# Performance work log

Hardware: AMD Instinct MI355X
Metric: run time of the kernel (lower is better)

The kernel has to match this reference:

```python
import jax, jax.numpy as jnp
import numpy as np

B, S, E, H = 4, 2048, 256, 8
D = E // H
SCALE = D ** -0.5


def setup_inputs() -> dict:
    key = jax.random.key(0)
    k1, k2, k3, k4, k5, k6 = jax.random.split(key, 6)
    x = jax.random.normal(k1, (B, S, E), dtype=jnp.float32)
    lengths = jax.random.randint(k2, (B,), S // 4, S + 1)
    # binary prefix mask, as assumed by mask[i].sum() == valid length in the original
    mask = (jnp.arange(S)[None, :] < lengths[:, None]).astype(jnp.int32)
    w_std = 1.0 / np.sqrt(E)
    Wq = jax.random.normal(k3, (E, E), dtype=jnp.float32) * w_std
    Wk = jax.random.normal(k4, (E, E), dtype=jnp.float32) * w_std
    Wv = jax.random.normal(k5, (E, E), dtype=jnp.float32) * w_std
    Wo = jax.random.normal(k6, (E, E), dtype=jnp.float32) * w_std
    return {"x": x, "mask": mask, "Wq": Wq, "Wk": Wk, "Wv": Wv, "Wo": Wo}


def _scramble_pad(attn_i, L):
    # attn_i: [S, H, D] attention output for one sample; only query rows < L are used.
    # Faithful to torch: attn[:L] viewed as [H, L, D] (after transpose(1,2)) then
    # reshape(L, E), zero-padded to [S, E]. The reshape mixes heads in a
    # length-dependent way, reproduced here with integer index arithmetic.
    L_safe = jnp.maximum(L, 1)
    flat = jnp.arange(S * E)                     # flat index into [H, L, D] row-major
    h = jnp.minimum(flat // (L_safe * D), H - 1)
    rem = flat % (L_safe * D)
    s = rem // D
    d = rem % D
    valid = flat < L * E
    vals = attn_i[s, h, d]
    return jnp.where(valid, vals, 0.0).reshape(S, E)


def reference(x, mask, Wq, Wk, Wv, Wo):
    # projections (torch Linear, no bias: y = x @ W.T), split heads
    Q = (x @ Wq.T).reshape(B, S, H, D)
    K = (x @ Wk.T).reshape(B, S, H, D)
    V = (x @ Wv.T).reshape(B, S, H, D)
    scores = jnp.einsum("bqhd,bkhd->bhqk", Q, K) * SCALE
    key_valid = mask[:, None, None, :] > 0       # prefix key mask == per-sample varlen attn
    scores = jnp.where(key_valid, scores, -1e30)
    P = jax.nn.softmax(scores, axis=-1)
    attn = jnp.einsum("bhqk,bkhd->bqhd", P, V)   # [B, S, H, D]
    lengths = mask.sum(axis=1)
    padded = jax.vmap(_scramble_pad)(attn, lengths)  # [B, S, E]
    return padded @ Wo.T
```

## Files before the change

kernel.cpp:

```cpp
#include <hip/hip_runtime.h>
#include <cmath>

#define Bn 4
#define Sn 2048
#define En 256
#define Hn 8
#define Dn 32
#define KD 256
#define NS 4
#define CHUNK 512

static constexpr float SCALE_LOG2E = 0.25504210472155044f;

typedef _Float16 half4_t __attribute__((ext_vector_type(4)));
typedef _Float16 half8_t __attribute__((ext_vector_type(8)));
typedef float float4_t __attribute__((ext_vector_type(4)));

__global__ __launch_bounds__(256) void cvt_kernel(
    const float* __restrict__ Wq, const float* __restrict__ Wk,
    const float* __restrict__ Wv, const float* __restrict__ Wo,
    const int* __restrict__ mask, _Float16* __restrict__ Wh,
    int* __restrict__ len) {
  if (blockIdx.x == 128) {
    const int b = threadIdx.x >> 6, lane = threadIdx.x & 63;
    int s = 0;
    for (int i = lane; i < Sn; i += 64) s += mask[b * Sn + i];
#pragma unroll
    for (int off = 32; off > 0; off >>= 1) s += __shfl_down(s, off, 64);
    if (lane == 0) len[b] = s;
    return;
  }
  const size_t wi = ((size_t)blockIdx.x * 256 + threadIdx.x) * 8;
  const int w = (int)(wi >> 16);
  const size_t off = wi & 65535;
  const float* src = (w == 0) ? Wq : (w == 1) ? Wk : (w == 2) ? Wv : Wo;
  float4 a = *(const float4*)&src[off];
  float4 b2 = *(const float4*)&src[off + 4];
  half8_t h;
  h[0] = (_Float16)a.x;  h[1] = (_Float16)a.y;
  h[2] = (_Float16)a.z;  h[3] = (_Float16)a.w;
  h[4] = (_Float16)b2.x; h[5] = (_Float16)b2.y;
  h[6] = (_Float16)b2.z; h[7] = (_Float16)b2.w;
  *(half8_t*)&(Wh + (size_t)w * 65536)[off] = h;
}

__global__ __launch_bounds__(256) void qkv_gemm(
    const float* __restrict__ x, const _Float16* __restrict__ Wh,
    _Float16* __restrict__ Qh, _Float16* __restrict__ Kh,
    _Float16* __restrict__ Vt) {
  const int lane = threadIdx.x & 63;
  const int wv = threadIdx.x >> 6;
  const int quad = lane >> 4, l15 = lane & 15;
  const int fid = blockIdx.x + 12 * blockIdx.y;
  const int wl = (fid & 7) * 48 + (fid >> 3);
  const int nb = wl % 12, mb = wl / 12;
  const int n0 = nb * 64;
  const int mw = mb * 256 + wv * 64;

  float4_t C[4][4];
#pragma unroll
  for (int i = 0; i < 4; ++i)
#pragma unroll
    for (int j = 0; j < 4; ++j) C[i][j] = (float4_t){0.f, 0.f, 0.f, 0.f};

  for (int k0 = 0; k0 < KD; k0 += 32) {
    half8_t A[4], Bf[4];
#pragma unroll
    for (int i = 0; i < 4; ++i) {
      const float4* xp =
          (const float4*)&x[(size_t)(mw + 16 * i + l15) * KD + k0 + quad * 8];
      const float4 a0 = xp[0], a1 = xp[1];
      A[i][0] = (_Float16)a0.x; A[i][1] = (_Float16)a0.y;
      A[i][2] = (_Float16)a0.z; A[i][3] = (_Float16)a0.w;
      A[i][4] = (_Float16)a1.x; A[i][5] = (_Float16)a1.y;
      A[i][6] = (_Float16)a1.z; A[i][7] = (_Float16)a1.w;
    }
#pragma unroll
    for (int j = 0; j < 4; ++j)
      Bf[j] = *(const half8_t*)&Wh[(size_t)(n0 + 16 * j + l15) * KD + k0 + quad * 8];
#pragma unroll
    for (int i = 0; i < 4; ++i)
#pragma unroll
      for (int j = 0; j < 4; ++j)
        C[i][j] = __builtin_amdgcn_mfma_f32_16x16x32_f16(A[i], Bf[j], C[i][j], 0, 0, 0);
  }

  const int mat = n0 >> 8;
  if (mat < 2) {
    _Float16* dstH = mat ? Kh : Qh;
    const float scale = mat ? 1.0f : SCALE_LOG2E;
#pragma unroll
    for (int i = 0; i < 4; ++i)
#pragma unroll
      for (int j = 0; j < 4; ++j) {
        const int c = ((n0 + 16 * j) & 255) + l15;
        const int h = c >> 5, d = c & 31;
#pragma unroll
        for (int r = 0; r < 4; ++r) {
          const int m = mw + 16 * i + quad * 4 + r;
          const int b = m >> 11, s = m & (Sn - 1);
          dstH[((size_t)(b * Hn + h) * Sn + s) * Dn + d] =
              (_Float16)(C[i][j][r] * scale);
        }
      }
  } else {
#pragma unroll
    for (int i = 0; i < 4; ++i)
#pragma unroll
      for (int j = 0; j < 4; ++j) {
        const int c = ((n0 + 16 * j) & 255) + l15;
        const int h = c >> 5, d = c & 31;
        const int m = mw + 16 * i + quad * 4;
        const int b = m >> 11, s = m & (Sn - 1);
        half4_t hv;
#pragma unroll
        for (int r = 0; r < 4; ++r) hv[r] = (_Float16)C[i][j][r];
        *(half4_t*)&Vt[(size_t)(b * Hn + h) * (Sn * Dn) +
                       (size_t)(s >> 5) * 1024 + d * 32 + (s & 31)] = hv;
      }
  }
}

__global__ __launch_bounds__(256) void out_gemm(
    const _Float16* __restrict__ Ph, const _Float16* __restrict__ Woh,
    float* __restrict__ out) {
  const int lane = threadIdx.x & 63;
  const int wv = threadIdx.x >> 6;
  const int quad = lane >> 4, l15 = lane & 15;
  const int fid = blockIdx.x + 4 * blockIdx.y;
  const int wl = (fid & 7) * 16 + (fid >> 3);
  const int nb = wl % 4, mb = wl / 4;
  const int n0 = nb * 64;
  const int mw = mb * 256 + wv * 64;

  float4_t C[4][4];
#pragma unroll
  for (int i = 0; i < 4; ++i)
#pragma unroll
    for (int j = 0; j < 4; ++j) C[i][j] = (float4_t){0.f, 0.f, 0.f, 0.f};

  for (int k0 = 0; k0 < KD; k0 += 32) {
    half8_t A[4], Bf[4];
#pragma unroll
    for (int i = 0; i < 4; ++i)
      A[i] = *(const half8_t*)&Ph[(size_t)(mw + 16 * i + l15) * KD + k0 + quad * 8];
#pragma unroll
    for (int j = 0; j < 4; ++j)
      Bf[j] = *(const half8_t*)&Woh[(size_t)(n0 + 16 * j + l15) * KD + k0 + quad * 8];
#pragma unroll
    for (int i = 0; i < 4; ++i)
#pragma unroll
      for (int j = 0; j < 4; ++j)
        C[i][j] = __builtin_amdgcn_mfma_f32_16x16x32_f16(A[i], Bf[j], C[i][j], 0, 0, 0);
  }

#pragma unroll
  for (int i = 0; i < 4; ++i)
#pragma unroll
    for (int j = 0; j < 4; ++j)
#pragma unroll
      for (int r = 0; r < 4; ++r)
        out[(size_t)(mw + 16 * i + quad * 4 + r) * En + n0 + 16 * j + l15] =
            C[i][j][r];
}

__global__ __launch_bounds__(256) void attn_kernel(
    const _Float16* __restrict__ Qh, const _Float16* __restrict__ Kh,
    const _Float16* __restrict__ Vt, const int* __restrict__ len,
    _Float16* __restrict__ pacc, float* __restrict__ pl) {
  const int lid = blockIdx.x + 32 * (blockIdx.y + 8 * blockIdx.z);
  const int h = lid & 7;
  const int w = lid >> 3;
  const int b = w >> 5;
  const int inner = w & 31;
  const int split = inner & (NS - 1);
  const int qg = inner >> 2;

  const int L = len[b];
  const int lane = threadIdx.x & 63;
  const int wv = threadIdx.x >> 6;
  const int q0 = (qg * 4 + wv) * 64;
  if (q0 >= L) return;
  const int ks = split * CHUNK;
  if (ks >= L) return;
  const int ke = min(L, ks + CHUNK);

  const int quad = lane >> 4;
  const int l15 = lane & 15;
  const size_t bh = (size_t)(b * Hn + h) * Sn;
  const _Float16* Vt0 = &Vt[(size_t)(b * Hn + h) * (Sn * Dn)];

  half8_t qf[4];
#pragma unroll
  for (int t = 0; t < 4; ++t)
    qf[t] = *(const half8_t*)&Qh[(bh + q0 + 16 * t + l15) * Dn + quad * 8];

  float4_t o0[4], o1[4];
  float ll[4];
#pragma unroll
  for (int t = 0; t < 4; ++t) {
    o0[t] = (float4_t){0.f, 0.f, 0.f, 0.f};
    o1[t] = (float4_t){0.f, 0.f, 0.f, 0.f};
    ll[t] = 0.f;
  }

  const int vo0 = l15 * 32 + quad * 4;
  const int vo1 = (l15 + 16) * 32 + quad * 4;

  const _Float16* vt_c = &Vt0[(size_t)(ks >> 5) * 1024];
  half8_t kfc0 = *(const half8_t*)&Kh[(bh + ks + l15) * Dn + quad * 8];
  half8_t kfc1 = *(const half8_t*)&Kh[(bh + ks + 16 + l15) * Dn + quad * 8];
  half4_t v0c = *(const half4_t*)&vt_c[vo0];
  half4_t v1c = *(const half4_t*)&vt_c[vo1];
  half4_t v2c = *(const half4_t*)&vt_c[vo0 + 16];
  half4_t v3c = *(const half4_t*)&vt_c[vo1 + 16];

  const int r1 = (ks + 32 < ke) ? ks + 32 : ks;
  const _Float16* vt_1 = &Vt0[(size_t)(r1 >> 5) * 1024];
  half8_t kfn0 = *(const half8_t*)&Kh[(bh + r1 + l15) * Dn + quad * 8];
  half8_t kfn1 = *(const half8_t*)&Kh[(bh + r1 + 16 + l15) * Dn + quad * 8];
  half4_t v0n = *(const half4_t*)&vt_1[vo0];
  half4_t v1n = *(const half4_t*)&vt_1[vo1];
  half4_t v2n = *(const half4_t*)&vt_1[vo0 + 16];
  half4_t v3n = *(const half4_t*)&vt_1[vo1 + 16];

  for (int k0 = ks; k0 < ke; k0 += 32) {
    const int kp = k0 + 64;
    const int kn = (kp < ke) ? kp : ks;
    const _Float16* vt_t = &Vt0[(size_t)(kn >> 5) * 1024];
    const half8_t kft0 = *(const half8_t*)&Kh[(bh + kn + l15) * Dn + quad * 8];
    const half8_t kft1 = *(const half8_t*)&Kh[(bh + kn + 16 + l15) * Dn + quad * 8];
    const half4_t v0t = *(const half4_t*)&vt_t[vo0];
    const half4_t v1t = *(const half4_t*)&vt_t[vo1];
    const half4_t v2t = *(const half4_t*)&vt_t[vo0 + 16];
    const half4_t v3t = *(const half4_t*)&vt_t[vo1 + 16];

    __builtin_amdgcn_s_setprio(1);
    float4_t st0[4], st1[4];
#pragma unroll
    for (int t = 0; t < 4; ++t) {
      st0[t] = (float4_t){0.f, 0.f, 0.f, 0.f};
      st1[t] = (float4_t){0.f, 0.f, 0.f, 0.f};
      st0[t] = __builtin_amdgcn_mfma_f32_16x16x32_f16(kfc0, qf[t], st0[t], 0, 0, 0);
      st1[t] = __builtin_amdgcn_mfma_f32_16x16x32_f16(kfc1, qf[t], st1[t], 0, 0, 0);
    }

    if (k0 + 32 <= ke) {
#pragma unroll
      for (int t = 0; t < 4; ++t) {
        half4_t pf0, pf1;
#pragma unroll
        for (int r = 0; r < 4; ++r) {
          const float pa = __builtin_amdgcn_exp2f(st0[t][r]);
          const float pb = __builtin_amdgcn_exp2f(st1[t][r]);
          ll[t] += pa + pb;
          pf0[r] = (_Float16)pa;
          pf1[r] = (_Float16)pb;
        }
        o0[t] = __builtin_amdgcn_mfma_f32_16x16x16f16(pf0, v0c, o0[t], 0, 0, 0);
        o1[t] = __builtin_amdgcn_mfma_f32_16x16x16f16(pf0, v1c, o1[t], 0, 0, 0);
        o0[t] = __builtin_amdgcn_mfma_f32_16x16x16f16(pf1, v2c, o0[t], 0, 0, 0);
        o1[t] = __builtin_amdgcn_mfma_f32_16x16x16f16(pf1, v3c, o1[t], 0, 0, 0);
      }
    } else {
      const int ka = k0 + quad * 4, kb = k0 + 16 + quad * 4;
#pragma unroll
      for (int t = 0; t < 4; ++t) {
        half4_t pf0, pf1;
#pragma unroll
        for (int r = 0; r < 4; ++r) {
          const float pa = __builtin_amdgcn_exp2f((ka + r < ke) ? st0[t][r] : -3.0e38f);
          const float pb = __builtin_amdgcn_exp2f((kb + r < ke) ? st1[t][r] : -3.0e38f);
          ll[t] += pa + pb;
          pf0[r] = (_Float16)pa;
          pf1[r] = (_Float16)pb;
        }
        o0[t] = __builtin_amdgcn_mfma_f32_16x16x16f16(pf0, v0c, o0[t], 0, 0, 0);
        o1[t] = __builtin_amdgcn_mfma_f32_16x16x16f16(pf0, v1c, o1[t], 0, 0, 0);
        o0[t] = __builtin_amdgcn_mfma_f32_16x16x16f16(pf1, v2c, o0[t], 0, 0, 0);
        o1[t] = __builtin_amdgcn_mfma_f32_16x16x16f16(pf1, v3c, o1[t], 0, 0, 0);
      }
    }
    __builtin_amdgcn_s_setprio(0);
    kfc0 = kfn0; kfc1 = kfn1;
    v0c = v0n; v1c = v1n; v2c = v2n; v3c = v3n;
    kfn0 = kft0; kfn1 = kft1;
    v0n = v0t; v1n = v1t; v2n = v2t; v3n = v3t;
  }

#pragma unroll
  for (int t = 0; t < 4; ++t) {
    ll[t] += __shfl_xor(ll[t], 16);
    ll[t] += __shfl_xor(ll[t], 32);
  }

  const size_t idx0 = ((size_t)(b * Hn + h) * NS + split) * Sn + q0;
#pragma unroll
  for (int t = 0; t < 4; ++t) {
#pragma unroll
    for (int r = 0; r < 4; ++r) {
      _Float16* pp = &pacc[(idx0 + 16 * t + quad * 4 + r) * 32];
      pp[l15] = (_Float16)o0[t][r];
      pp[l15 + 16] = (_Float16)o1[t][r];
    }
  }
  if (quad == 0) {
#pragma unroll
    for (int t = 0; t < 4; ++t) pl[idx0 + 16 * t + l15] = ll[t];
  }
}

__global__ __launch_bounds__(256) void combine_kernel(const _Float16* __restrict__ pacc,
                                                      const float* __restrict__ pl,
                                                      const int* __restrict__ len,
                                                      _Float16* __restrict__ Ph) {
  const int b = blockIdx.z;
  const int L = len[b];
  if (blockIdx.y == Hn) {
    _Float16* base = Ph + (size_t)b * Sn * En;
    const size_t end = (size_t)Sn * En;
    const size_t stride = (size_t)gridDim.x * 256 * 8;
    half8_t z = {0, 0, 0, 0, 0, 0, 0, 0};
    for (size_t idx = (size_t)L * En + ((size_t)blockIdx.x * 256 + threadIdx.x) * 8;
         idx < end; idx += stride)
      *(half8_t*)&base[idx] = z;
    return;
  }
  const int h = blockIdx.y;
  const int q = blockIdx.x * 256 + threadIdx.x;
  if (q >= L) return;
  const size_t base = (size_t)(b * Hn + h) * NS * Sn;

  float T = 0.f;
  float o[32];
#pragma unroll
  for (int d = 0; d < 32; ++d) o[d] = 0.f;
#pragma unroll
  for (int sp = 0; sp < NS; ++sp) {
    if (sp * CHUNK < L) {
      T += pl[base + (size_t)sp * Sn + q];
      const half8_t* pp = (const half8_t*)&pacc[(base + (size_t)sp * Sn + q) * 32];
#pragma unroll
      for (int i = 0; i < 4; ++i) {
        half8_t v = pp[i];
#pragma unroll
        for (int t2 = 0; t2 < 8; ++t2) o[i * 8 + t2] += (float)v[t2];
      }
    }
  }
  const float inv = 1.0f / T;
  _Float16* dst = &Ph[(size_t)b * Sn * En + (size_t)h * L * Dn + (size_t)q * Dn];
#pragma unroll
  for (int i = 0; i < 4; ++i) {
    half8_t hv;
#pragma unroll
    for (int t2 = 0; t2 < 8; ++t2) hv[t2] = (_Float16)(o[i * 8 + t2] * inv);
    *(half8_t*)&dst[i * 8] = hv;
  }
}

extern "C" void kernel_launch(void* const* d_in, const int* in_sizes, int n_in,
                              void* d_out, int out_size, void* d_ws, size_t ws_size,
                              hipStream_t stream) {
  (void)in_sizes; (void)n_in; (void)out_size; (void)ws_size;
  const float* x  = (const float*)d_in[0];
  const int* mask = (const int*)d_in[1];
  const float* Wq = (const float*)d_in[2];
  const float* Wk = (const float*)d_in[3];
  const float* Wv = (const float*)d_in[4];
  const float* Wo = (const float*)d_in[5];
  float* out = (float*)d_out;

  float* wsf = (float*)d_ws;
  int* lengths = (int*)d_ws;
  const size_t BHSD = (size_t)Bn * Hn * Sn * Dn;
  _Float16* Wh = (_Float16*)(wsf + 64);
  _Float16* Qh = Wh + 4 * 65536;
  _Float16* Kh = Qh + BHSD;
  _Float16* Vt = Kh + BHSD;
  _Float16* Ph = Vt + BHSD;
  _Float16* pacc = Ph + BHSD;
  float* pl = (float*)(pacc + (size_t)Bn * Hn * NS * Sn * 32);

  cvt_kernel<<<dim3(129), 256, 0, stream>>>(Wq, Wk, Wv, Wo, mask, Wh, lengths);
  qkv_gemm<<<dim3(12, 32), 256, 0, stream>>>(x, Wh, Qh, Kh, Vt);
  attn_kernel<<<dim3((Sn / 256) * NS, Hn, Bn), 256, 0, stream>>>(
      Qh, Kh, Vt, lengths, pacc, pl);
  combine_kernel<<<dim3(Sn / 256, Hn + 1, Bn), 256, 0, stream>>>(
      pacc, pl, lengths, Ph);
  out_gemm<<<dim3(4, 32), 256, 0, stream>>>(Ph, Wh + 3 * 65536, out);
}
```

Baseline: 143.4 us.

## Stage K/V tiles through swizzled LDS shared by all waves via direct loads

The attention kernel now double-buffers each 32-key K and V tile in shared memory using global_load_lds. Each of the four waves loads one quarter of the tile, and all waves in the block then read the whole tile from LDS instead of each fetching it from global memory separately. The projection kernel writes K and Vt with an XOR swizzle so the LDS fragment reads avoid bank conflicts. Waves whose query rows lie past the valid length still take part in staging and barriers, which adds two block barriers per tile and some idle wave work.

Measured after the change: 143.0 us. About the same (-0.3%).

```diff
diff --git a/kernel.cpp b/kernel.cpp
--- a/kernel.cpp
+++ b/kernel.cpp
@@ -86,9 +86,7 @@
   }
 
   const int mat = n0 >> 8;
-  if (mat < 2) {
-    _Float16* dstH = mat ? Kh : Qh;
-    const float scale = mat ? 1.0f : SCALE_LOG2E;
+  if (mat == 0) {
 #pragma unroll
     for (int i = 0; i < 4; ++i)
 #pragma unroll
@@ -99,8 +97,24 @@
         for (int r = 0; r < 4; ++r) {
           const int m = mw + 16 * i + quad * 4 + r;
           const int b = m >> 11, s = m & (Sn - 1);
-          dstH[((size_t)(b * Hn + h) * Sn + s) * Dn + d] =
-              (_Float16)(C[i][j][r] * scale);
+          Qh[((size_t)(b * Hn + h) * Sn + s) * Dn + d] =
+              (_Float16)(C[i][j][r] * SCALE_LOG2E);
+        }
+      }
+  } else if (mat == 1) {
+#pragma unroll
+    for (int i = 0; i < 4; ++i)
+#pragma unroll
+      for (int j = 0; j < 4; ++j) {
+        const int c = ((n0 + 16 * j) & 255) + l15;
+        const int h = c >> 5, d = c & 31;
+        const int g = d >> 3, dl = d & 7;
+#pragma unroll
+        for (int r = 0; r < 4; ++r) {
+          const int m = mw + 16 * i + quad * 4 + r;
+          const int b = m >> 11, s = m & (Sn - 1);
+          Kh[((size_t)(b * Hn + h) * Sn + s) * Dn + ((g ^ (s & 3)) << 3) + dl] =
+              (_Float16)C[i][j][r];
         }
       }
   } else {
@@ -112,11 +126,12 @@
         const int h = c >> 5, d = c & 31;
         const int m = mw + 16 * i + quad * 4;
         const int b = m >> 11, s = m & (Sn - 1);
+        const int g = (((s & 31) >> 3) ^ (d & 3)) << 3;
         half4_t hv;
 #pragma unroll
         for (int r = 0; r < 4; ++r) hv[r] = (_Float16)C[i][j][r];
         *(half4_t*)&Vt[(size_t)(b * Hn + h) * (Sn * Dn) +
-                       (size_t)(s >> 5) * 1024 + d * 32 + (s & 31)] = hv;
+                       (size_t)(s >> 5) * 1024 + d * 32 + g + (s & 7)] = hv;
       }
   }
 }
@@ -177,23 +192,29 @@
   const int qg = inner >> 2;
 
   const int L = len[b];
+  const int ks = split * CHUNK;
+  if (ks >= L) return;
+  const int ke = min(L, ks + CHUNK);
+  const int nr = (ke - ks + 31) >> 5;
+
   const int lane = threadIdx.x & 63;
   const int wv = threadIdx.x >> 6;
   const int q0 = (qg * 4 + wv) * 64;
-  if (q0 >= L) return;
-  const int ks = split * CHUNK;
-  if (ks >= L) return;
-  const int ke = min(L, ks + CHUNK);
+  const bool act = (q0 < L);
 
   const int quad = lane >> 4;
   const int l15 = lane & 15;
   const size_t bh = (size_t)(b * Hn + h) * Sn;
   const _Float16* Vt0 = &Vt[(size_t)(b * Hn + h) * (Sn * Dn)];
 
+  __shared__ char smem[8192] __attribute__((aligned(128)));
+
   half8_t qf[4];
-#pragma unroll
-  for (int t = 0; t < 4; ++t)
-    qf[t] = *(const half8_t*)&Qh[(bh + q0 + 16 * t + l15) * Dn + quad * 8];
+  if (act) {
+#pragma unroll
+    for (int t = 0; t < 4; ++t)
+      qf[t] = *(const half8_t*)&Qh[(bh + q0 + 16 * t + l15) * Dn + quad * 8];
+  }
 
   float4_t o0[4], o1[4];
   float ll[4];
@@ -204,89 +225,94 @@
     ll[t] = 0.f;
   }
 
-  const int vo0 = l15 * 32 + quad * 4;
-  const int vo1 = (l15 + 16) * 32 + quad * 4;
-
-  const _Float16* vt_c = &Vt0[(size_t)(ks >> 5) * 1024];
-  half8_t kfc0 = *(const half8_t*)&Kh[(bh + ks + l15) * Dn + quad * 8];
-  half8_t kfc1 = *(const half8_t*)&Kh[(bh + ks + 16 + l15) * Dn + quad * 8];
-  half4_t v0c = *(const half4_t*)&vt_c[vo0];
-  half4_t v1c = *(const half4_t*)&vt_c[vo1];
-  half4_t v2c = *(const half4_t*)&vt_c[vo0 + 16];
-  half4_t v3c = *(const half4_t*)&vt_c[vo1 + 16];
-
-  const int r1 = (ks + 32 < ke) ? ks + 32 : ks;
-  const _Float16* vt_1 = &Vt0[(size_t)(r1 >> 5) * 1024];
-  half8_t kfn0 = *(const half8_t*)&Kh[(bh + r1 + l15) * Dn + quad * 8];
-  half8_t kfn1 = *(const half8_t*)&Kh[(bh + r1 + 16 + l15) * Dn + quad * 8];
-  half4_t v0n = *(const half4_t*)&vt_1[vo0];
-  half4_t v1n = *(const half4_t*)&vt_1[vo1];
-  half4_t v2n = *(const half4_t*)&vt_1[vo0 + 16];
-  half4_t v3n = *(const half4_t*)&vt_1[vo1 + 16];
-
-  for (int k0 = ks; k0 < ke; k0 += 32) {
-    const int kp = k0 + 64;
-    const int kn = (kp < ke) ? kp : ks;
-    const _Float16* vt_t = &Vt0[(size_t)(kn >> 5) * 1024];
-    const half8_t kft0 = *(const half8_t*)&Kh[(bh + kn + l15) * Dn + quad * 8];
-    const half8_t kft1 = *(const half8_t*)&Kh[(bh + kn + 16 + l15) * Dn + quad * 8];
-    const half4_t v0t = *(const half4_t*)&vt_t[vo0];
-    const half4_t v1t = *(const half4_t*)&vt_t[vo1];
-    const half4_t v2t = *(const half4_t*)&vt_t[vo0 + 16];
-    const half4_t v3t = *(const half4_t*)&vt_t[vo1 + 16];
-
-    __builtin_amdgcn_s_setprio(1);
-    float4_t st0[4], st1[4];
-#pragma unroll
-    for (int t = 0; t < 4; ++t) {
-      st0[t] = (float4_t){0.f, 0.f, 0.f, 0.f};
-      st1[t] = (float4_t){0.f, 0.f, 0.f, 0.f};
-      st0[t] = __builtin_amdgcn_mfma_f32_16x16x32_f16(kfc0, qf[t], st0[t], 0, 0, 0);
-      st1[t] = __builtin_amdgcn_mfma_f32_16x16x32_f16(kfc1, qf[t], st1[t], 0, 0, 0);
+  const int swK = (quad ^ (l15 & 3)) << 4;
+  const int gV0 = (((quad >> 1) ^ (l15 & 3)) << 4) + ((quad & 1) << 3);
+  const int gV2 = ((((quad >> 1) + 2) ^ (l15 & 3)) << 4) + ((quad & 1) << 3);
+
+#define STAGE(bufsel, kk)                                                      \
+  do {                                                                         \
+    const char* gK_ = (const char*)(Kh + (bh + (kk)) * Dn);                    \
+    const char* gV_ = (const char*)(Vt0 + (size_t)((kk) >> 5) * 1024);         \
+    const char* src_ = (wv < 2) ? (gK_ + wv * 1024) : (gV_ + (wv - 2) * 1024); \
+    __builtin_amdgcn_global_load_lds(                                          \
+        (const __attribute__((address_space(1))) void*)(src_ + lane * 16),     \
+        (__attribute__((address_space(3))) void*)&smem[(bufsel) * 4096 +       \
+                                                       wv * 1024],             \
+        16, 0, 0);                                                             \
+  } while (0)
+
+  STAGE(0, ks);
+  int cur = 0;
+
+  for (int r = 0; r < nr; ++r) {
+    const int k0 = ks + (r << 5);
+    const int kn = (k0 + 32 < ke) ? (k0 + 32) : ks;
+    STAGE(cur ^ 1, kn);
+    asm volatile("s_waitcnt vmcnt(1)" ::: "memory");
+    __builtin_amdgcn_s_barrier();
+
+    if (act) {
+      const char* sK = &smem[cur * 4096];
+      const char* sV = &smem[cur * 4096 + 2048];
+      const half8_t kfc0 = *(const half8_t*)&sK[l15 * 64 + swK];
+      const half8_t kfc1 = *(const half8_t*)&sK[(l15 + 16) * 64 + swK];
+      const half4_t v0c = *(const half4_t*)&sV[l15 * 64 + gV0];
+      const half4_t v1c = *(const half4_t*)&sV[(l15 + 16) * 64 + gV0];
+      const half4_t v2c = *(const half4_t*)&sV[l15 * 64 + gV2];
+      const half4_t v3c = *(const half4_t*)&sV[(l15 + 16) * 64 + gV2];
+
+      float4_t st0[4], st1[4];
+#pragma unroll
+      for (int t = 0; t < 4; ++t) {
+        st0[t] = (float4_t){0.f, 0.f, 0.f, 0.f};
+        st1[t] = (float4_t){0.f, 0.f, 0.f, 0.f};
+        st0[t] = __builtin_amdgcn_mfma_f32_16x16x32_f16(kfc0, qf[t], st0[t], 0, 0, 0);
+        st1[t] = __builtin_amdgcn_mfma_f32_16x16x32_f16(kfc1, qf[t], st1[t], 0, 0, 0);
+      }
+
+      if (k0 + 32 <= ke) {
+#pragma unroll
+        for (int t = 0; t < 4; ++t) {
+          half4_t pf0, pf1;
+#pragma unroll
+          for (int r2 = 0; r2 < 4; ++r2) {
+            const float pa = __builtin_amdgcn_exp2f(st0[t][r2]);
+            const float pb = __builtin_amdgcn_exp2f(st1[t][r2]);
+            ll[t] += pa + pb;
+            pf0[r2] = (_Float16)pa;
+            pf1[r2] = (_Float16)pb;
+          }
+          o0[t] = __builtin_amdgcn_mfma_f32_16x16x16f16(pf0, v0c, o0[t], 0, 0, 0);
+          o1[t] = __builtin_amdgcn_mfma_f32_16x16x16f16(pf0, v1c, o1[t], 0, 0, 0);
+          o0[t] = __builtin_amdgcn_mfma_f32_16x16x16f16(pf1, v2c, o0[t], 0, 0, 0);
+          o1[t] = __builtin_amdgcn_mfma_f32_16x16x16f16(pf1, v3c, o1[t], 0, 0, 0);
+        }
+      } else {
+        const int ka = k0 + quad * 4, kb = k0 + 16 + quad * 4;
+#pragma unroll
+        for (int t = 0; t < 4; ++t) {
+          half4_t pf0, pf1;
+#pragma unroll
+          for (int r2 = 0; r2 < 4; ++r2) {
+            const float pa = __builtin_amdgcn_exp2f((ka + r2 < ke) ? st0[t][r2] : -3.0e38f);
+            const float pb = __builtin_amdgcn_exp2f((kb + r2 < ke) ? st1[t][r2] : -3.0e38f);
+            ll[t] += pa + pb;
+            pf0[r2] = (_Float16)pa;
+            pf1[r2] = (_Float16)pb;
+          }
+          o0[t] = __builtin_amdgcn_mfma_f32_16x16x16f16(pf0, v0c, o0[t], 0, 0, 0);
+          o1[t] = __builtin_amdgcn_mfma_f32_16x16x16f16(pf0, v1c, o1[t], 0, 0, 0);
+          o0[t] = __builtin_amdgcn_mfma_f32_16x16x16f16(pf1, v2c, o0[t], 0, 0, 0);
+          o1[t] = __builtin_amdgcn_mfma_f32_16x16x16f16(pf1, v3c, o1[t], 0, 0, 0);
+        }
+      }
     }
-
-    if (k0 + 32 <= ke) {
-#pragma unroll
-      for (int t = 0; t < 4; ++t) {
-        half4_t pf0, pf1;
-#pragma unroll
-        for (int r = 0; r < 4; ++r) {
-          const float pa = __builtin_amdgcn_exp2f(st0[t][r]);
-          const float pb = __builtin_amdgcn_exp2f(st1[t][r]);
-          ll[t] += pa + pb;
-          pf0[r] = (_Float16)pa;
-          pf1[r] = (_Float16)pb;
-        }
-        o0[t] = __builtin_amdgcn_mfma_f32_16x16x16f16(pf0, v0c, o0[t], 0, 0, 0);
-        o1[t] = __builtin_amdgcn_mfma_f32_16x16x16f16(pf0, v1c, o1[t], 0, 0, 0);
-        o0[t] = __builtin_amdgcn_mfma_f32_16x16x16f16(pf1, v2c, o0[t], 0, 0, 0);
-        o1[t] = __builtin_amdgcn_mfma_f32_16x16x16f16(pf1, v3c, o1[t], 0, 0, 0);
-      }
-    } else {
-      const int ka = k0 + quad * 4, kb = k0 + 16 + quad * 4;
-#pragma unroll
-      for (int t = 0; t < 4; ++t) {
-        half4_t pf0, pf1;
-#pragma unroll
-        for (int r = 0; r < 4; ++r) {
-          const float pa = __builtin_amdgcn_exp2f((ka + r < ke) ? st0[t][r] : -3.0e38f);
-          const float pb = __builtin_amdgcn_exp2f((kb + r < ke) ? st1[t][r] : -3.0e38f);
-          ll[t] += pa + pb;
-          pf0[r] = (_Float16)pa;
-          pf1[r] = (_Float16)pb;
-        }
-        o0[t] = __builtin_amdgcn_mfma_f32_16x16x16f16(pf0, v0c, o0[t], 0, 0, 0);
-        o1[t] = __builtin_amdgcn_mfma_f32_16x16x16f16(pf0, v1c, o1[t], 0, 0, 0);
-        o0[t] = __builtin_amdgcn_mfma_f32_16x16x16f16(pf1, v2c, o0[t], 0, 0, 0);
-        o1[t] = __builtin_amdgcn_mfma_f32_16x16x16f16(pf1, v3c, o1[t], 0, 0, 0);
-      }
-    }
-    __builtin_amdgcn_s_setprio(0);
-    kfc0 = kfn0; kfc1 = kfn1;
-    v0c = v0n; v1c = v1n; v2c = v2n; v3c = v3n;
-    kfn0 = kft0; kfn1 = kft1;
-    v0n = v0t; v1n = v1t; v2n = v2t; v3n = v3t;
-  }
+    __builtin_amdgcn_s_barrier();
+    cur ^= 1;
+  }
+#undef STAGE
+
+  if (!act) return;
 
 #pragma unroll
   for (int t = 0; t < 4; ++t) {
```

## Process 64 keys per attention loop iteration with single-stage register prefetch

Applied to the files above, without the earlier changes.

The attention inner loop now handles two 32-key sub-blocks per iteration. It prefetches the next 64 keys' K and V fragments one iteration ahead, replacing the two-deep rotating prefetch of 32-key tiles. The s_setprio priority hints are removed. This halves loop overhead and register rotation per key but shortens the prefetch distance and may raise register pressure. The tail handling also now assumes the 64-key tile's second half is readable even when only partly valid.

New measurement: 138.0 us. 3.7% less time.

```diff
diff --git a/kernel.cpp b/kernel.cpp
--- a/kernel.cpp
+++ b/kernel.cpp
@@ -207,45 +207,45 @@
   const int vo0 = l15 * 32 + quad * 4;
   const int vo1 = (l15 + 16) * 32 + quad * 4;
 
-  const _Float16* vt_c = &Vt0[(size_t)(ks >> 5) * 1024];
+  const _Float16* vtA = &Vt0[(size_t)(ks >> 5) * 1024];
   half8_t kfc0 = *(const half8_t*)&Kh[(bh + ks + l15) * Dn + quad * 8];
   half8_t kfc1 = *(const half8_t*)&Kh[(bh + ks + 16 + l15) * Dn + quad * 8];
-  half4_t v0c = *(const half4_t*)&vt_c[vo0];
-  half4_t v1c = *(const half4_t*)&vt_c[vo1];
-  half4_t v2c = *(const half4_t*)&vt_c[vo0 + 16];
-  half4_t v3c = *(const half4_t*)&vt_c[vo1 + 16];
-
-  const int r1 = (ks + 32 < ke) ? ks + 32 : ks;
-  const _Float16* vt_1 = &Vt0[(size_t)(r1 >> 5) * 1024];
-  half8_t kfn0 = *(const half8_t*)&Kh[(bh + r1 + l15) * Dn + quad * 8];
-  half8_t kfn1 = *(const half8_t*)&Kh[(bh + r1 + 16 + l15) * Dn + quad * 8];
-  half4_t v0n = *(const half4_t*)&vt_1[vo0];
-  half4_t v1n = *(const half4_t*)&vt_1[vo1];
-  half4_t v2n = *(const half4_t*)&vt_1[vo0 + 16];
-  half4_t v3n = *(const half4_t*)&vt_1[vo1 + 16];
-
-  for (int k0 = ks; k0 < ke; k0 += 32) {
-    const int kp = k0 + 64;
-    const int kn = (kp < ke) ? kp : ks;
-    const _Float16* vt_t = &Vt0[(size_t)(kn >> 5) * 1024];
-    const half8_t kft0 = *(const half8_t*)&Kh[(bh + kn + l15) * Dn + quad * 8];
-    const half8_t kft1 = *(const half8_t*)&Kh[(bh + kn + 16 + l15) * Dn + quad * 8];
-    const half4_t v0t = *(const half4_t*)&vt_t[vo0];
-    const half4_t v1t = *(const half4_t*)&vt_t[vo1];
-    const half4_t v2t = *(const half4_t*)&vt_t[vo0 + 16];
-    const half4_t v3t = *(const half4_t*)&vt_t[vo1 + 16];
-
-    __builtin_amdgcn_s_setprio(1);
+  half8_t kfc2 = *(const half8_t*)&Kh[(bh + ks + 32 + l15) * Dn + quad * 8];
+  half8_t kfc3 = *(const half8_t*)&Kh[(bh + ks + 48 + l15) * Dn + quad * 8];
+  half4_t v0c = *(const half4_t*)&vtA[vo0];
+  half4_t v1c = *(const half4_t*)&vtA[vo1];
+  half4_t v2c = *(const half4_t*)&vtA[vo0 + 16];
+  half4_t v3c = *(const half4_t*)&vtA[vo1 + 16];
+  half4_t v4c = *(const half4_t*)&vtA[1024 + vo0];
+  half4_t v5c = *(const half4_t*)&vtA[1024 + vo1];
+  half4_t v6c = *(const half4_t*)&vtA[1024 + vo0 + 16];
+  half4_t v7c = *(const half4_t*)&vtA[1024 + vo1 + 16];
+
+  for (int k0 = ks; k0 < ke; k0 += 64) {
+    const int kn = (k0 + 64 < ke) ? k0 + 64 : ks;
+    const _Float16* vtN = &Vt0[(size_t)(kn >> 5) * 1024];
+    const half8_t kfn0 = *(const half8_t*)&Kh[(bh + kn + l15) * Dn + quad * 8];
+    const half8_t kfn1 = *(const half8_t*)&Kh[(bh + kn + 16 + l15) * Dn + quad * 8];
+    const half8_t kfn2 = *(const half8_t*)&Kh[(bh + kn + 32 + l15) * Dn + quad * 8];
+    const half8_t kfn3 = *(const half8_t*)&Kh[(bh + kn + 48 + l15) * Dn + quad * 8];
+    const half4_t v0n = *(const half4_t*)&vtN[vo0];
+    const half4_t v1n = *(const half4_t*)&vtN[vo1];
+    const half4_t v2n = *(const half4_t*)&vtN[vo0 + 16];
+    const half4_t v3n = *(const half4_t*)&vtN[vo1 + 16];
+    const half4_t v4n = *(const half4_t*)&vtN[1024 + vo0];
+    const half4_t v5n = *(const half4_t*)&vtN[1024 + vo1];
+    const half4_t v6n = *(const half4_t*)&vtN[1024 + vo0 + 16];
+    const half4_t v7n = *(const half4_t*)&vtN[1024 + vo1 + 16];
+
     float4_t st0[4], st1[4];
-#pragma unroll
-    for (int t = 0; t < 4; ++t) {
-      st0[t] = (float4_t){0.f, 0.f, 0.f, 0.f};
-      st1[t] = (float4_t){0.f, 0.f, 0.f, 0.f};
-      st0[t] = __builtin_amdgcn_mfma_f32_16x16x32_f16(kfc0, qf[t], st0[t], 0, 0, 0);
-      st1[t] = __builtin_amdgcn_mfma_f32_16x16x32_f16(kfc1, qf[t], st1[t], 0, 0, 0);
-    }
-
-    if (k0 + 32 <= ke) {
+    if (k0 + 64 <= ke) {
+#pragma unroll
+      for (int t = 0; t < 4; ++t) {
+        st0[t] = (float4_t){0.f, 0.f, 0.f, 0.f};
+        st1[t] = (float4_t){0.f, 0.f, 0.f, 0.f};
+        st0[t] = __builtin_amdgcn_mfma_f32_16x16x32_f16(kfc0, qf[t], st0[t], 0, 0, 0);
+        st1[t] = __builtin_amdgcn_mfma_f32_16x16x32_f16(kfc1, qf[t], st1[t], 0, 0, 0);
+      }
 #pragma unroll
       for (int t = 0; t < 4; ++t) {
         half4_t pf0, pf1;
@@ -262,8 +262,38 @@
         o0[t] = __builtin_amdgcn_mfma_f32_16x16x16f16(pf1, v2c, o0[t], 0, 0, 0);
         o1[t] = __builtin_amdgcn_mfma_f32_16x16x16f16(pf1, v3c, o1[t], 0, 0, 0);
       }
+#pragma unroll
+      for (int t = 0; t < 4; ++t) {
+        st0[t] = (float4_t){0.f, 0.f, 0.f, 0.f};
+        st1[t] = (float4_t){0.f, 0.f, 0.f, 0.f};
+        st0[t] = __builtin_amdgcn_mfma_f32_16x16x32_f16(kfc2, qf[t], st0[t], 0, 0, 0);
+        st1[t] = __builtin_amdgcn_mfma_f32_16x16x32_f16(kfc3, qf[t], st1[t], 0, 0, 0);
+      }
+#pragma unroll
+      for (int t = 0; t < 4; ++t) {
+        half4_t pf0, pf1;
+#pragma unroll
+        for (int r = 0; r < 4; ++r) {
+          const float pa = __builtin_amdgcn_exp2f(st0[t][r]);
+          const float pb = __builtin_amdgcn_exp2f(st1[t][r]);
+          ll[t] += pa + pb;
+          pf0[r] = (_Float16)pa;
+          pf1[r] = (_Float16)pb;
+        }
+        o0[t] = __builtin_amdgcn_mfma_f32_16x16x16f16(pf0, v4c, o0[t], 0, 0, 0);
+        o1[t] = __builtin_amdgcn_mfma_f32_16x16x16f16(pf0, v5c, o1[t], 0, 0, 0);
+        o0[t] = __builtin_amdgcn_mfma_f32_16x16x16f16(pf1, v6c, o0[t], 0, 0, 0);
+        o1[t] = __builtin_amdgcn_mfma_f32_16x16x16f16(pf1, v7c, o1[t], 0, 0, 0);
+      }
     } else {
       const int ka = k0 + quad * 4, kb = k0 + 16 + quad * 4;
+#pragma unroll
+      for (int t = 0; t < 4; ++t) {
+        st0[t] = (float4_t){0.f, 0.f, 0.f, 0.f};
+        st1[t] = (float4_t){0.f, 0.f, 0.f, 0.f};
+        st0[t] = __builtin_amdgcn_mfma_f32_16x16x32_f16(kfc0, qf[t], st0[t], 0, 0, 0);
+        st1[t] = __builtin_amdgcn_mfma_f32_16x16x32_f16(kfc1, qf[t], st1[t], 0, 0, 0);
+      }
 #pragma unroll
       for (int t = 0; t < 4; ++t) {
         half4_t pf0, pf1;
@@ -280,12 +310,36 @@
         o0[t] = __builtin_amdgcn_mfma_f32_16x16x16f16(pf1, v2c, o0[t], 0, 0, 0);
         o1[t] = __builtin_amdgcn_mfma_f32_16x16x16f16(pf1, v3c, o1[t], 0, 0, 0);
       }
+      if (k0 + 32 < ke) {
+        const int kc = k0 + 32 + quad * 4, kd = k0 + 48 + quad * 4;
+#pragma unroll
+        for (int t = 0; t < 4; ++t) {
+          st0[t] = (float4_t){0.f, 0.f, 0.f, 0.f};
+          st1[t] = (float4_t){0.f, 0.f, 0.f, 0.f};
+          st0[t] = __builtin_amdgcn_mfma_f32_16x16x32_f16(kfc2, qf[t], st0[t], 0, 0, 0);
+          st1[t] = __builtin_amdgcn_mfma_f32_16x16x32_f16(kfc3, qf[t], st1[t], 0, 0, 0);
+        }
+#pragma unroll
+        for (int t = 0; t < 4; ++t) {
+          half4_t pf0, pf1;
+#pragma unroll
+          for (int r = 0; r < 4; ++r) {
+            const float pa = __builtin_amdgcn_exp2f((kc + r < ke) ? st0[t][r] : -3.0e38f);
+            const float pb = __builtin_amdgcn_exp2f((kd + r < ke) ? st1[t][r] : -3.0e38f);
+            ll[t] += pa + pb;
+            pf0[r] = (_Float16)pa;
+            pf1[r] = (_Float16)pb;
+          }
+          o0[t] = __builtin_amdgcn_mfma_f32_16x16x16f16(pf0, v4c, o0[t], 0, 0, 0);
+          o1[t] = __builtin_amdgcn_mfma_f32_16x16x16f16(pf0, v5c, o1[t], 0, 0, 0);
+          o0[t] = __builtin_amdgcn_mfma_f32_16x16x16f16(pf1, v6c, o0[t], 0, 0, 0);
+          o1[t] = __builtin_amdgcn_mfma_f32_16x16x16f16(pf1, v7c, o1[t], 0, 0, 0);
+        }
+      }
     }
-    __builtin_amdgcn_s_setprio(0);
-    kfc0 = kfn0; kfc1 = kfn1;
+    kfc0 = kfn0; kfc1 = kfn1; kfc2 = kfn2; kfc3 = kfn3;
     v0c = v0n; v1c = v1n; v2c = v2n; v3c = v3n;
-    kfn0 = kft0; kfn1 = kft1;
-    v0n = v0t; v1n = v1t; v2n = v2t; v3n = v3t;
+    v4c = v4n; v5c = v5n; v6c = v6n; v7c = v7n;
   }
 
 #pragma unroll
```
